# Kernel tuning notes

Hardware: AMD Instinct MI355X
Metric: run time of the kernel (lower is better)

The kernel has to match this reference:

```python
import jax, jax.numpy as jnp
import numpy as np

H = 16      # num_attention_heads
HKV = 4     # num_key_value_heads
HIDDEN = 1024
HEAD_DIM = HIDDEN // H  # 64
ROPE_BASE = 10000.0


def _rope(x):
    # Rotate-half RoPE applied over the FULL projected last dim, matching the
    # module which applies self._rope before splitting into heads.
    B, S, D = x.shape
    half = D // 2
    inv_freq = 1.0 / (ROPE_BASE ** (jnp.arange(half, dtype=jnp.float32) / half))
    ang = jnp.arange(S, dtype=jnp.float32)[:, None] * inv_freq[None, :]  # [S, half]
    cos, sin = jnp.cos(ang), jnp.sin(ang)
    x1, x2 = x[..., :half], x[..., half:]
    return jnp.concatenate([x1 * cos - x2 * sin, x2 * cos + x1 * sin], axis=-1)


def _rmsnorm(x):
    # F.rms_norm with no weight: x / sqrt(mean(x^2) + eps)
    eps = jnp.finfo(x.dtype).eps
    return x * jax.lax.rsqrt(jnp.mean(x * x, axis=-1, keepdims=True) + eps)


def setup_inputs() -> dict:
    key = jax.random.key(0)
    ks = jax.random.split(key, 10)
    B, S = 2, 2048
    kv_dim = HKV * HEAD_DIM
    sc = 0.02
    return {
        "hidden_state": jax.random.normal(ks[0], (B, S, HIDDEN), dtype=jnp.float32),
        "attention_mask": jnp.zeros((B, S, S), dtype=jnp.float32),
        "Wq": jax.random.normal(ks[1], (HIDDEN, HIDDEN), dtype=jnp.float32) * sc,
        "bq": jnp.zeros((HIDDEN,), dtype=jnp.float32),
        "Wk": jax.random.normal(ks[2], (HIDDEN, kv_dim), dtype=jnp.float32) * sc,
        "bk": jnp.zeros((kv_dim,), dtype=jnp.float32),
        "Wv": jax.random.normal(ks[3], (HIDDEN, kv_dim), dtype=jnp.float32) * sc,
        "bv": jnp.zeros((kv_dim,), dtype=jnp.float32),
        "Wo": jax.random.normal(ks[4], (HIDDEN, HIDDEN), dtype=jnp.float32) * sc,
        "bo": jnp.zeros((HIDDEN,), dtype=jnp.float32),
    }


def reference(hidden_state, attention_mask, Wq, bq, Wk, bk, Wv, bv, Wo, bo):
    B, S, _ = hidden_state.shape
    G = H // HKV  # query heads per kv head
    d = HEAD_DIM

    q = hidden_state @ Wq + bq            # [B,S,H*d]
    k = hidden_state @ Wk + bk            # [B,S,Hkv*d]
    v = hidden_state @ Wv + bv            # [B,S,Hkv*d]

    q = _rope(q)
    k = _rope(k)

    # split heads; repeat_interleave of KV over groups == grouping Q heads as [Hkv, G]
    q = q.reshape(B, S, H, d).transpose(0, 2, 1, 3).reshape(B, HKV, G, S, d)
    k = k.reshape(B, S, HKV, d).transpose(0, 2, 1, 3)   # [B,Hkv,S,d]
    v = v.reshape(B, S, HKV, d).transpose(0, 2, 1, 3)   # [B,Hkv,S,d]

    q = _rmsnorm(q)
    k = _rmsnorm(k)

    scale = d ** 0.5
    scores = jnp.einsum('bkgqd,bksd->bkgqs', q, k) / scale  # [B,Hkv,G,S,S]
    scores = scores + attention_mask[:, None, None, :, :]
    attn = jax.nn.softmax(scores, axis=-1)
    out = jnp.einsum('bkgqs,bksd->bkgqd', attn, v)          # [B,Hkv,G,S,d]

    out = out.reshape(B, H, S, d).transpose(0, 2, 1, 3).reshape(B, S, H * d)
    return out @ Wo + bo
```

## Files before the change

kernel.cpp:

```cpp
#include <hip/hip_runtime.h>
#include <cmath>

#define SEQ 2048
#define BATCH 2
#define HID 1024
#define NH 16
#define NKV 4
#define DH 64
#define KVDIM 256
#define K32C 32

typedef __attribute__((ext_vector_type(8))) short bf16x8;
typedef __attribute__((ext_vector_type(4))) float f32x4;

static __device__ __forceinline__ unsigned short f2bf(float x) {
  union { float f; unsigned u; } v; v.f = x;
  unsigned r = v.u + 0x7fffu + ((v.u >> 16) & 1u);
  return (unsigned short)(r >> 16);
}
static __device__ __forceinline__ float bf2f(unsigned short h) {
  union { unsigned u; float f; } v; v.u = ((unsigned)h) << 16;
  return v.f;
}
static __device__ __forceinline__ void gl_lds16(const void* g, void* l) {
  __builtin_amdgcn_global_load_lds(
      (const __attribute__((address_space(1))) unsigned int*)g,
      (__attribute__((address_space(3))) unsigned int*)l, 16, 0, 0);
}

template<bool HILO>
static __device__ __forceinline__ void pack_a_body(
    const float* __restrict__ A, unsigned short* __restrict__ hi,
    unsigned short* __restrict__ lo, int lbid) {
  int gid = lbid * 256 + threadIdx.x;
  int lane = gid & 63;
  int k32 = (gid >> 6) & 31;
  int m16 = gid >> 11;
  int quad = lane >> 4, l16 = lane & 15;
  const float* src = A + (size_t)(m16 * 16 + l16) * 1024 + k32 * 32 + quad * 8;
  float4 a0 = *(const float4*)src;
  float4 a1 = *(const float4*)(src + 4);
  float v[8] = {a0.x, a0.y, a0.z, a0.w, a1.x, a1.y, a1.z, a1.w};
  unsigned short h[8], l[8];
#pragma unroll
  for (int j = 0; j < 8; ++j) {
    h[j] = f2bf(v[j]);
    if (HILO) l[j] = f2bf(v[j] - bf2f(h[j]));
  }
  *(bf16x8*)(hi + (size_t)gid * 8) = *(bf16x8*)h;
  if (HILO) *(bf16x8*)(lo + (size_t)gid * 8) = *(bf16x8*)l;
}

template<bool HILO>
static __device__ __forceinline__ void pack_b_body(
    const float* __restrict__ W, unsigned short* __restrict__ hi,
    unsigned short* __restrict__ lo, int Nsrc, int lbid) {
  int gid = lbid * 256 + threadIdx.x;
  int lane = gid & 63;
  int k32 = (gid >> 6) & 31;
  int n16 = gid >> 11;
  int quad = lane >> 4, l16 = lane & 15;
  int n = n16 * 16 + l16, k = k32 * 32 + quad * 8;
  unsigned short h[8], l[8];
#pragma unroll
  for (int j = 0; j < 8; ++j) {
    float v = W[(size_t)(k + j) * Nsrc + n];
    h[j] = f2bf(v);
    if (HILO) l[j] = f2bf(v - bf2f(h[j]));
  }
  *(bf16x8*)(hi + (size_t)gid * 8) = *(bf16x8*)h;
  if (HILO) *(bf16x8*)(lo + (size_t)gid * 8) = *(bf16x8*)l;
}

template<bool HILO>
__global__ __launch_bounds__(256) void pack_a_kernel(
    const float* __restrict__ A, unsigned short* __restrict__ hi,
    unsigned short* __restrict__ lo) {
  pack_a_body<HILO>(A, hi, lo, blockIdx.x);
}

__global__ __launch_bounds__(256) void prep_pack_kernel(
    const float* __restrict__ hs, const float* __restrict__ Wq,
    const float* __restrict__ Wk, const float* __restrict__ Wv,
    const float* __restrict__ Wo, const float* __restrict__ bq,
    const float* __restrict__ bk, const float* __restrict__ bv,
    unsigned short* __restrict__ hs_pk, unsigned short* __restrict__ Wqkv_hi,
    unsigned short* __restrict__ Wo_hi, unsigned short* __restrict__ Wo_lo,
    float* __restrict__ bias_c) {
  const int bid = blockIdx.x;
  if (bid < 2048) {
    pack_a_body<false>(hs, hs_pk, nullptr, bid);
  } else if (bid < 2560) {
    pack_b_body<false>(Wq, Wqkv_hi, nullptr, 1024, bid - 2048);
  } else if (bid < 2688) {
    pack_b_body<false>(Wk, Wqkv_hi + (size_t)64 * 2048 * 8, nullptr, 256, bid - 2560);
  } else if (bid < 2816) {
    pack_b_body<false>(Wv, Wqkv_hi + (size_t)80 * 2048 * 8, nullptr, 256, bid - 2688);
  } else if (bid < 3328) {
    pack_b_body<true>(Wo, Wo_hi, Wo_lo, 1024, bid - 2816);
  } else {
    int n = (bid - 3328) * 256 + threadIdx.x;
    if (n < 1536)
      bias_c[n] = (n < 1024) ? bq[n] : (n < 1280 ? bk[n - 1024] : bv[n - 1280]);
  }
}

template<int CHAINS, bool OUTBF16>
__global__ __launch_bounds__(256) void gemm_pk_kernel(
    const unsigned short* __restrict__ Ah, const unsigned short* __restrict__ Al,
    const unsigned short* __restrict__ Bh, const unsigned short* __restrict__ Bl,
    const float* __restrict__ bias, void* __restrict__ Cout, int N) {
  constexpr int NCH = (CHAINS == 3) ? 2 : 1;
  __shared__ unsigned short Asm[NCH][4 * 512];
  __shared__ unsigned short Bsm[NCH][8 * 512];
  const int tid = threadIdx.x;
  const int wave = tid >> 6, lane = tid & 63;
  const int wr = wave >> 1, wc = wave & 1;
  const int quad = lane >> 4, l16 = lane & 15;
  const size_t abase = ((size_t)(blockIdx.y * 4 + wave) * K32C) * 64 + lane;
  const size_t bbase0 = ((size_t)(blockIdx.x * 8 + wave) * K32C) * 64 + lane;
  const size_t bbase1 = ((size_t)(blockIdx.x * 8 + wave + 4) * K32C) * 64 + lane;
  f32x4 acc[2][4] = {};
  for (int k32 = 0; k32 < K32C; ++k32) {
    __syncthreads();
    gl_lds16(Ah + (abase + (size_t)k32 * 64) * 8, &Asm[0][wave * 512]);
    gl_lds16(Bh + (bbase0 + (size_t)k32 * 64) * 8, &Bsm[0][wave * 512]);
    gl_lds16(Bh + (bbase1 + (size_t)k32 * 64) * 8, &Bsm[0][(wave + 4) * 512]);
    if (CHAINS == 3) {
      gl_lds16(Al + (abase + (size_t)k32 * 64) * 8, &Asm[1][wave * 512]);
      gl_lds16(Bl + (bbase0 + (size_t)k32 * 64) * 8, &Bsm[1][wave * 512]);
      gl_lds16(Bl + (bbase1 + (size_t)k32 * 64) * 8, &Bsm[1][(wave + 4) * 512]);
    }
    __syncthreads();
    bf16x8 af[2][NCH], bfr[4][NCH];
#pragma unroll
    for (int mt = 0; mt < 2; ++mt)
#pragma unroll
      for (int ch = 0; ch < NCH; ++ch)
        af[mt][ch] = *(const bf16x8*)&Asm[ch][((wr * 2 + mt) * 64 + lane) * 8];
#pragma unroll
    for (int nt = 0; nt < 4; ++nt)
#pragma unroll
      for (int ch = 0; ch < NCH; ++ch)
        bfr[nt][ch] = *(const bf16x8*)&Bsm[ch][((wc * 4 + nt) * 64 + lane) * 8];
#pragma unroll
    for (int mt = 0; mt < 2; ++mt)
#pragma unroll
      for (int nt = 0; nt < 4; ++nt) {
        acc[mt][nt] = __builtin_amdgcn_mfma_f32_16x16x32_bf16(af[mt][0], bfr[nt][0], acc[mt][nt], 0, 0, 0);
        if (CHAINS == 3) {
          acc[mt][nt] = __builtin_amdgcn_mfma_f32_16x16x32_bf16(af[mt][1], bfr[nt][0], acc[mt][nt], 0, 0, 0);
          acc[mt][nt] = __builtin_amdgcn_mfma_f32_16x16x32_bf16(af[mt][0], bfr[nt][1], acc[mt][nt], 0, 0, 0);
        }
      }
  }
  const int n0 = blockIdx.x * 128 + wc * 64;
  const int m0 = blockIdx.y * 64 + wr * 32;
#pragma unroll
  for (int mt = 0; mt < 2; ++mt)
#pragma unroll
    for (int nt = 0; nt < 4; ++nt)
#pragma unroll
      for (int r = 0; r < 4; ++r) {
        int gm = m0 + mt * 16 + quad * 4 + r;
        int n = n0 + nt * 16 + l16;
        float v = acc[mt][nt][r] + bias[n];
        if (OUTBF16)
          ((unsigned short*)Cout)[(size_t)gm * N + n] = f2bf(v);
        else
          ((float*)Cout)[(size_t)gm * N + n] = v;
      }
}

__global__ __launch_bounds__(1024) void rope_norm_kernel(
    const unsigned short* __restrict__ qkv, unsigned short* __restrict__ Qh,
    unsigned short* __restrict__ Ql, unsigned short* __restrict__ Kpk,
    unsigned short* __restrict__ Vpk) {
  const int s = blockIdx.x, b = blockIdx.y;
  const int t = threadIdx.x;
  const unsigned short* row = qkv + ((size_t)b * SEQ + s) * 1536;
  {
    const int j = t & 511;
    float invf = exp2f((float)j * (-13.287712379549449f / 512.0f));
    float ang = (float)s * invf;
    float c = cosf(ang), sn = sinf(ang);
    float x1 = bf2f(row[j]), x2 = bf2f(row[j + 512]);
    float val = (t < 512) ? (x1 * c - x2 * sn) : (x2 * c + x1 * sn);
    float ss = val * val;
#pragma unroll
    for (int off = 1; off < 64; off <<= 1) ss += __shfl_xor(ss, off);
    float rn = rsqrtf(ss * (1.0f / 64.0f) + 1.1920929e-07f);
    float v = val * rn;
    unsigned short hi = f2bf(v);
    unsigned short lo = f2bf(v - bf2f(hi));
    int h = t >> 6, d = t & 63;
    size_t o = (size_t)(b * NH + h) * 131072 +
               ((((size_t)(s >> 4) * 2 + (d >> 5)) * 64) + ((d >> 3) & 3) * 16 + (s & 15)) * 8 + (d & 7);
    Qh[o] = hi;
    Ql[o] = lo;
  }
  if (t < 256) {
    const int j = t & 127;
    float invf = exp2f((float)j * (-13.287712379549449f / 128.0f));
    float ang = (float)s * invf;
    float c = cosf(ang), sn = sinf(ang);
    float x1 = bf2f(row[1024 + j]), x2 = bf2f(row[1024 + 128 + j]);
    float val = (t < 128) ? (x1 * c - x2 * sn) : (x2 * c + x1 * sn);
    float ss = val * val;
#pragma unroll
    for (int off = 1; off < 64; off <<= 1) ss += __shfl_xor(ss, off);
    float rn = rsqrtf(ss * (1.0f / 64.0f) + 1.1920929e-07f);
    float kv = val * rn;
    int h = t >> 6, d = t & 63;
    size_t ko = (size_t)(b * NKV + h) * 131072 +
                ((((size_t)(s >> 4) * 2 + (d >> 5)) * 64) + ((d >> 3) & 3) * 16 + (s & 15)) * 8 + (d & 7);
    Kpk[ko] = f2bf(kv);
  } else if (t < 512) {
    const int tv = t - 256;
    int h = tv >> 6, d = tv & 63;
    size_t vo = (size_t)(b * NKV + h) * 131072 +
                ((((size_t)(d >> 4) * 64 + (s >> 5)) * 64) + ((s >> 3) & 3) * 16 + (d & 15)) * 8 + (s & 7);
    Vpk[vo] = row[1280 + tv];
  }
}

__global__ __launch_bounds__(512, 4) void attn_mfma6_kernel(
    const unsigned short* __restrict__ Qh, const unsigned short* __restrict__ Ql,
    const unsigned short* __restrict__ Kpk, const unsigned short* __restrict__ Vpk,
    const float* __restrict__ mask, float* __restrict__ attn_o) {
  __shared__ __align__(16) char smem[67584];
  unsigned short* Kb = (unsigned short*)smem;
  unsigned short* Vb = (unsigned short*)(smem + 16384);
  float*          Msk = (float*)(smem + 32768);
  unsigned short* Ps = (unsigned short*)(smem + 49152);

  const int b = blockIdx.z, kvh = blockIdx.y;
  const int q0 = blockIdx.x * 32;
  const int tid = threadIdx.x, wave = tid >> 6, lane = tid & 63;
  const int jh = wave >> 2, w4 = wave & 3;
  const int quad = lane >> 4, l16 = lane & 15;
  const int h = kvh * 4 + w4;

  bf16x8 qh[2][2], ql[2][2];
  {
    const unsigned short* Qb_h = Qh + (size_t)(b * NH + h) * 131072;
    const unsigned short* Qb_l = Ql + (size_t)(b * NH + h) * 131072;
#pragma unroll
    for (int mt = 0; mt < 2; ++mt)
#pragma unroll
      for (int kf = 0; kf < 2; ++kf) {
        size_t o = ((((size_t)(q0 >> 4) + mt) * 2 + kf) * 64 + lane) * 8;
        qh[mt][kf] = *(const bf16x8*)(Qb_h + o);
        ql[mt][kf] = *(const bf16x8*)(Qb_l + o);
      }
  }

  const unsigned short* Kbase = Kpk + (size_t)(b * NKV + kvh) * 131072;
  const unsigned short* Vbase = Vpk + (size_t)(b * NKV + kvh) * 131072;

  const float* mbase = mask + ((size_t)b * SEQ + q0) * SEQ;
  const int srow = w4 * 8 + (lane >> 3);
  const int ssw = ((srow >> 2) & 1) << 4;
  const float* msrc0 = mbase + (size_t)srow * SEQ + (((lane & 7) * 4) ^ ssw);

  bf16x8 ones;
#pragma unroll
  for (int i = 0; i < 8; ++i) ones[i] = (short)0x3F80;

  f32x4 O[2][4] = {};
  f32x4 lAcc[2] = {};

  auto stage = [&](int buf, int jc) {
    const int j0 = jh * (SEQ / 2) + jc * 32;
    gl_lds16(Kbase + ((((size_t)(j0 >> 4) + (w4 >> 1)) * 2 + (w4 & 1)) * 64 + lane) * 8,
             Kb + (buf * 2 + jh) * 2048 + w4 * 512);
    gl_lds16(Vbase + (((size_t)w4 * 64 + (j0 >> 5)) * 64 + lane) * 8,
             Vb + (buf * 2 + jh) * 2048 + w4 * 512);
    gl_lds16(msrc0 + j0, Msk + (buf * 2 + jh) * 1024 + w4 * 256);
  };

  stage(0, 0);
  for (int jc = 0; jc < 32; ++jc) {
    const int cur = jc & 1;
    __syncthreads();
    if (jc < 31) stage(cur ^ 1, jc + 1);

    bf16x8 kbf[2][2], vbf[4];
#pragma unroll
    for (int nt = 0; nt < 2; ++nt)
#pragma unroll
      for (int kf = 0; kf < 2; ++kf)
        kbf[nt][kf] = *(const bf16x8*)&Kb[(cur * 2 + jh) * 2048 + ((nt * 2 + kf) * 64 + lane) * 8];
#pragma unroll
    for (int d16 = 0; d16 < 4; ++d16)
      vbf[d16] = *(const bf16x8*)&Vb[(cur * 2 + jh) * 2048 + (d16 * 64 + lane) * 8];

    bf16x8 pa[2];
#pragma unroll
    for (int mt = 0; mt < 2; ++mt) {
#pragma unroll
      for (int nt = 0; nt < 2; ++nt) {
        f32x4 C = {};
        C = __builtin_amdgcn_mfma_f32_16x16x32_bf16(qh[mt][0], kbf[nt][0], C, 0, 0, 0);
        C = __builtin_amdgcn_mfma_f32_16x16x32_bf16(qh[mt][1], kbf[nt][1], C, 0, 0, 0);
        C = __builtin_amdgcn_mfma_f32_16x16x32_bf16(ql[mt][0], kbf[nt][0], C, 0, 0, 0);
        C = __builtin_amdgcn_mfma_f32_16x16x32_bf16(ql[mt][1], kbf[nt][1], C, 0, 0, 0);
#pragma unroll
        for (int r = 0; r < 4; ++r) {
          int row16 = quad * 4 + r;
          float m = Msk[(cur * 2 + jh) * 1024 + (mt * 16 + row16) * 32 +
                        ((nt * 16 + l16) ^ ((quad & 1) << 4))];
          float p = __builtin_amdgcn_exp2f(
              fmaf(C[r], 0.18033688f, fmaf(m, 1.44269504f, -11.54156033f)));
          union { float f; unsigned u; } pu; pu.f = p;
          Ps[wave * 1152 + row16 * 72 + nt * 16 + l16] =
              (unsigned short)((pu.u + 0x8000u) >> 16);
        }
      }
      pa[mt] = *(const bf16x8*)&Ps[wave * 1152 + l16 * 72 + quad * 8];
    }
#pragma unroll
    for (int mt = 0; mt < 2; ++mt) {
      lAcc[mt] = __builtin_amdgcn_mfma_f32_16x16x32_bf16(pa[mt], ones, lAcc[mt], 0, 0, 0);
#pragma unroll
      for (int nt = 0; nt < 4; ++nt)
        O[mt][nt] = __builtin_amdgcn_mfma_f32_16x16x32_bf16(pa[mt], vbf[nt], O[mt][nt], 0, 0, 0);
    }
  }

  __syncthreads();
  float* Oex = (float*)smem;
  float* lex = (float*)(smem + 34816);
  if (jh == 1) {
#pragma unroll
    for (int mt = 0; mt < 2; ++mt)
#pragma unroll
      for (int r = 0; r < 4; ++r) {
        int row = mt * 16 + quad * 4 + r;
#pragma unroll
        for (int nt = 0; nt < 4; ++nt)
          Oex[((size_t)w4 * 32 + row) * 68 + nt * 16 + l16] = O[mt][nt][r];
        if (l16 == 0) lex[w4 * 32 + row] = lAcc[mt][r];
      }
  }
  __syncthreads();
  if (jh == 0) {
    float* po = attn_o + ((size_t)b * SEQ + q0) * HID + h * DH;
#pragma unroll
    for (int mt = 0; mt < 2; ++mt)
#pragma unroll
      for (int r = 0; r < 4; ++r) {
        int row = mt * 16 + quad * 4 + r;
        float inv = 1.0f / (lAcc[mt][r] + lex[w4 * 32 + row]);
#pragma unroll
        for (int nt = 0; nt < 4; ++nt) {
          float v = (O[mt][nt][r] + Oex[((size_t)w4 * 32 + row) * 68 + nt * 16 + l16]) * inv;
          po[(size_t)row * HID + nt * 16 + l16] = v;
        }
      }
  }
}

extern "C" void kernel_launch(void* const* d_in, const int* in_sizes, int n_in,
                              void* d_out, int out_size, void* d_ws, size_t ws_size,
                              hipStream_t stream) {
  const float* hs   = (const float*)d_in[0];
  const float* mask = (const float*)d_in[1];
  const float* Wq   = (const float*)d_in[2];
  const float* bq   = (const float*)d_in[3];
  const float* Wk   = (const float*)d_in[4];
  const float* bk   = (const float*)d_in[5];
  const float* Wv   = (const float*)d_in[6];
  const float* bv   = (const float*)d_in[7];
  const float* Wo   = (const float*)d_in[8];
  const float* bo   = (const float*)d_in[9];
  float* out = (float*)d_out;
  char* ws = (char*)d_ws;
  const size_t MiB = 1048576;

  unsigned short* Wo_hi   = (unsigned short*)(ws);
  unsigned short* Wo_lo   = (unsigned short*)(ws + 2 * MiB);
  unsigned short* hs_pk   = (unsigned short*)(ws + 4 * MiB);
  unsigned short* Kpk     = (unsigned short*)(ws + 4 * MiB);
  unsigned short* Vpk     = (unsigned short*)(ws + 6 * MiB);
  float*          attn_o  = (float*)(ws + 8 * MiB);
  unsigned short* Wqkv_hi = (unsigned short*)(ws + 12 * MiB);
  float*          bias_c  = (float*)(ws + 15 * MiB);
  unsigned short* qkvproj = (unsigned short*)(ws + 16 * MiB);
  unsigned short* ao_hi   = (unsigned short*)(ws + 24 * MiB);
  unsigned short* Qpk_h   = (unsigned short*)(ws + 28 * MiB);
  unsigned short* ao_lo   = (unsigned short*)(ws + 32 * MiB);
  unsigned short* Qpk_l   = (unsigned short*)(ws + 36 * MiB);

  prep_pack_kernel<<<3334, 256, 0, stream>>>(
      hs, Wq, Wk, Wv, Wo, bq, bk, bv, hs_pk, Wqkv_hi, Wo_hi, Wo_lo, bias_c);

  gemm_pk_kernel<1, true><<<dim3(12, 64), 256, 0, stream>>>(
      hs_pk, nullptr, Wqkv_hi, nullptr, bias_c, qkvproj, 1536);

  rope_norm_kernel<<<dim3(SEQ, BATCH), dim3(1024), 0, stream>>>(
      qkvproj, Qpk_h, Qpk_l, Kpk, Vpk);

  attn_mfma6_kernel<<<dim3(SEQ / 32, NKV, BATCH), dim3(512), 0, stream>>>(
      Qpk_h, Qpk_l, Kpk, Vpk, mask, attn_o);

  pack_a_kernel<true><<<2048, 256, 0, stream>>>(attn_o, ao_hi, ao_lo);

  gemm_pk_kernel<3, false><<<dim3(8, 64), 256, 0, stream>>>(
      ao_hi, ao_lo, Wo_hi, Wo_lo, bo, out, 1024);
}
```

Before: 254.7 us.

## Load K, V and mask directly from global memory instead of LDS staging

Removes the double-buffered LDS staging of K, V and mask tiles and the per-iteration block barrier. Each wave now reads its K/V fragments and mask values straight from global memory into registers, and LDS shrinks to just the P scratch buffer. The aim is to cut barrier stalls and LDS traffic and to allow more resident blocks. The cost is that the four waves sharing a KV head each fetch the same K/V data separately, and global-load latency is no longer hidden by explicit prefetch.

```diff
diff --git a/kernel.cpp b/kernel.cpp
--- a/kernel.cpp
+++ b/kernel.cpp
@@ -224,15 +224,12 @@
   }
 }
 
-__global__ __launch_bounds__(512, 4) void attn_mfma6_kernel(
+__global__ __launch_bounds__(512, 4) void attn_mfma8_kernel(
     const unsigned short* __restrict__ Qh, const unsigned short* __restrict__ Ql,
     const unsigned short* __restrict__ Kpk, const unsigned short* __restrict__ Vpk,
     const float* __restrict__ mask, float* __restrict__ attn_o) {
-  __shared__ __align__(16) char smem[67584];
-  unsigned short* Kb = (unsigned short*)smem;
-  unsigned short* Vb = (unsigned short*)(smem + 16384);
-  float*          Msk = (float*)(smem + 32768);
-  unsigned short* Ps = (unsigned short*)(smem + 49152);
+  __shared__ __align__(16) char smem[35328];
+  unsigned short* Ps = (unsigned short*)smem;
 
   const int b = blockIdx.z, kvh = blockIdx.y;
   const int q0 = blockIdx.x * 32;
@@ -255,13 +252,18 @@
       }
   }
 
-  const unsigned short* Kbase = Kpk + (size_t)(b * NKV + kvh) * 131072;
-  const unsigned short* Vbase = Vpk + (size_t)(b * NKV + kvh) * 131072;
-
-  const float* mbase = mask + ((size_t)b * SEQ + q0) * SEQ;
-  const int srow = w4 * 8 + (lane >> 3);
-  const int ssw = ((srow >> 2) & 1) << 4;
-  const float* msrc0 = mbase + (size_t)srow * SEQ + (((lane & 7) * 4) ^ ssw);
+  const int jbase = jh * (SEQ / 2);
+  const unsigned short* kp0 = Kpk + (size_t)(b * NKV + kvh) * 131072 +
+                              ((size_t)(jbase >> 4) * 2 * 64 + lane) * 8;
+  const unsigned short* vp0 = Vpk + (size_t)(b * NKV + kvh) * 131072 +
+                              ((size_t)(jbase >> 5) * 64 + lane) * 8;
+  const float* mrow = mask + ((size_t)b * SEQ + q0) * SEQ + jbase + l16;
+  int moff[2][4];
+#pragma unroll
+  for (int mt = 0; mt < 2; ++mt)
+#pragma unroll
+    for (int r = 0; r < 4; ++r)
+      moff[mt][r] = (mt * 16 + quad * 4 + r) * SEQ;
 
   bf16x8 ones;
 #pragma unroll
@@ -270,30 +272,16 @@
   f32x4 O[2][4] = {};
   f32x4 lAcc[2] = {};
 
-  auto stage = [&](int buf, int jc) {
-    const int j0 = jh * (SEQ / 2) + jc * 32;
-    gl_lds16(Kbase + ((((size_t)(j0 >> 4) + (w4 >> 1)) * 2 + (w4 & 1)) * 64 + lane) * 8,
-             Kb + (buf * 2 + jh) * 2048 + w4 * 512);
-    gl_lds16(Vbase + (((size_t)w4 * 64 + (j0 >> 5)) * 64 + lane) * 8,
-             Vb + (buf * 2 + jh) * 2048 + w4 * 512);
-    gl_lds16(msrc0 + j0, Msk + (buf * 2 + jh) * 1024 + w4 * 256);
-  };
-
-  stage(0, 0);
   for (int jc = 0; jc < 32; ++jc) {
-    const int cur = jc & 1;
-    __syncthreads();
-    if (jc < 31) stage(cur ^ 1, jc + 1);
-
     bf16x8 kbf[2][2], vbf[4];
 #pragma unroll
     for (int nt = 0; nt < 2; ++nt)
 #pragma unroll
       for (int kf = 0; kf < 2; ++kf)
-        kbf[nt][kf] = *(const bf16x8*)&Kb[(cur * 2 + jh) * 2048 + ((nt * 2 + kf) * 64 + lane) * 8];
+        kbf[nt][kf] = *(const bf16x8*)(kp0 + ((jc * 2 + nt) * 2 + kf) * 512);
 #pragma unroll
     for (int d16 = 0; d16 < 4; ++d16)
-      vbf[d16] = *(const bf16x8*)&Vb[(cur * 2 + jh) * 2048 + (d16 * 64 + lane) * 8];
+      vbf[d16] = *(const bf16x8*)(vp0 + d16 * 32768 + jc * 512);
 
     bf16x8 pa[2];
 #pragma unroll
@@ -308,8 +296,7 @@
 #pragma unroll
         for (int r = 0; r < 4; ++r) {
           int row16 = quad * 4 + r;
-          float m = Msk[(cur * 2 + jh) * 1024 + (mt * 16 + row16) * 32 +
-                        ((nt * 16 + l16) ^ ((quad & 1) << 4))];
+          float m = mrow[moff[mt][r] + jc * 32 + nt * 16];
           float p = __builtin_amdgcn_exp2f(
               fmaf(C[r], 0.18033688f, fmaf(m, 1.44269504f, -11.54156033f)));
           union { float f; unsigned u; } pu; pu.f = p;
@@ -401,7 +388,7 @@
   rope_norm_kernel<<<dim3(SEQ, BATCH), dim3(1024), 0, stream>>>(
       qkvproj, Qpk_h, Qpk_l, Kpk, Vpk);
 
-  attn_mfma6_kernel<<<dim3(SEQ / 32, NKV, BATCH), dim3(512), 0, stream>>>(
+  attn_mfma8_kernel<<<dim3(SEQ / 32, NKV, BATCH), dim3(512), 0, stream>>>(
       Qpk_h, Qpk_l, Kpk, Vpk, mask, attn_o);
 
   pack_a_kernel<true><<<2048, 256, 0, stream>>>(attn_o, ao_hi, ao_lo);
```

Result: slower. 283.2 us (+11.2%).
